# Optimization experiments

Hardware: AMD Instinct MI355X
Metric: run time of the kernel (lower is better)

Reference implementation:

```python
import jax, jax.numpy as jnp
import numpy as np

# Static config mirroring init_kwargs
B, N = 1, 5
DS = 4                      # downsample
IMG_H, IMG_W = 256 // DS, 704 // DS          # 64, 176
D0, DSTEP, ND = 1.0, 0.5, 88                 # depth grid [1, 45, 0.5]
X, Y, Z = 200, 200, 16                       # occ grid dims from x/y/z bounds
NUM_CLASS = 10
IGNORE = 9
XYZ_MIN = np.array([-100.0, -100.0, -3.0], np.float32)   # bounds in cell units
XYZ_MAX = np.array([100.0, 100.0, 13.0], np.float32)
OCC_RATIO = 2.5             # 1 / grid_size (0.4)


def _frustum():
    # matches torch.meshgrid(w, h, d, indexing='xy') -> shape (IMG_H, IMG_W, ND)
    h = jnp.arange(IMG_H, dtype=jnp.float32) + 0.5
    w = jnp.arange(IMG_W, dtype=jnp.float32) + 0.5
    d = D0 + DSTEP * jnp.arange(ND, dtype=jnp.float32)
    Hm, Wm, Dm = jnp.meshgrid(w, h, d, indexing='xy')
    return jnp.stack([Hm, Wm, Dm], axis=-1).reshape(-1, 3)  # (P, 3): x_pix, y_pix, depth


def _forward(cam2ego_rot, cam2ego_trans, cam2img, post_rots, post_trans, sem_OCC_map):
    coords = _frustum()                       # (P, 3)
    P = coords.shape[0]
    pix = jnp.concatenate([coords[:, :2], jnp.ones((P, 1), jnp.float32)], axis=1).T  # (3, P)
    ds = jnp.array([DS, DS, 1.0], jnp.float32).reshape(3, 1)
    # frustum -> camera pixel plane (undo image augmentation)
    cam_pts = pix[None, None] * ds - post_trans[..., None]                # (B,N,3,P)
    cam_pts = jnp.einsum('bnij,bnjp->bnip', jnp.linalg.inv(post_rots), cam_pts)
    # lift by depth and unproject
    cam_pts = cam_pts * coords[:, 2][None, None, None, :]
    cam_pts = jnp.einsum('bnij,bnjp->bnip', jnp.linalg.inv(cam2img), cam_pts)
    # camera -> ego
    ego = jnp.einsum('bnij,bnjp->bnip', cam2ego_rot, cam_pts) + cam2ego_trans[..., None]  # (B,N,3,P)

    ego_occ = ego * OCC_RATIO                 # ego coords in occ-cell units
    xyz_min = jnp.asarray(XYZ_MIN).reshape(1, 1, 3, 1)
    xyz_max = jnp.asarray(XYZ_MAX).reshape(1, 1, 3, 1)
    norm = (ego_occ - xyz_min) / (xyz_max - xyz_min) * 2.0 - 1.0
    occ_mask = jnp.all((norm >= -1.0) & (norm <= 1.0), axis=2)            # (B,N,P)

    grid = ego_occ - xyz_min                  # index-space coords (B,N,3,P)
    # semantic volume: softmax then argmax over class dim
    sem_idx = jnp.argmax(jax.nn.softmax(sem_OCC_map, axis=-1), axis=-1).astype(jnp.int32)  # (B,X,Y,Z)
    ix = jnp.clip(jnp.floor(grid[:, :, 0]).astype(jnp.int32), 0, X - 1)
    iy = jnp.clip(jnp.floor(grid[:, :, 1]).astype(jnp.int32), 0, Y - 1)
    iz = jnp.clip(jnp.floor(grid[:, :, 2]).astype(jnp.int32), 0, Z - 1)
    lin = (ix * Y + iy) * Z + iz                                           # (B,N,P)
    gathered = jnp.take_along_axis(sem_idx.reshape(B, -1), lin.reshape(B, -1), axis=1)
    gathered = gathered.reshape(B, N, P)
    render = jnp.where(occ_mask, gathered, IGNORE).reshape(B, N, IMG_H, IMG_W, ND)

    # first non-ignore value along depth
    first_idx = jnp.argmax((render != IGNORE).astype(jnp.int32), axis=-1)  # (B,N,H,W)
    sem_view = jnp.take_along_axis(render, first_idx[..., None], axis=-1)[..., 0]
    depth_map = D0 + DSTEP * first_idx.astype(jnp.float32)
    return sem_view, depth_map


def setup_inputs() -> dict:
    rng = np.random.default_rng(0)
    # camera looks along ego +x: rotation mapping cam z->ego x, cam x->-ego y, cam y->-ego z
    R0 = np.array([[0., 0., 1.], [-1., 0., 0.], [0., -1., 0.]], np.float32)
    cam2ego_rot = np.broadcast_to(R0, (B, N, 3, 3)).copy()
    cam2ego_rot += 0.01 * rng.standard_normal((B, N, 3, 3)).astype(np.float32)
    cam2ego_trans = (0.5 * rng.standard_normal((B, N, 3))).astype(np.float32)
    K = np.zeros((B, N, 3, 3), np.float32)
    K[..., 0, 0] = 700.0; K[..., 1, 1] = 700.0
    K[..., 0, 2] = 352.0; K[..., 1, 2] = 128.0; K[..., 2, 2] = 1.0
    post_rots = np.broadcast_to(np.eye(3, dtype=np.float32), (B, N, 3, 3)).copy()
    post_rots += 0.01 * rng.standard_normal((B, N, 3, 3)).astype(np.float32)
    post_trans = (0.1 * rng.standard_normal((B, N, 3))).astype(np.float32)
    bda = np.broadcast_to(np.eye(3, dtype=np.float32), (B, 3, 3)).copy()
    sem_OCC_map = rng.standard_normal((B, X, Y, Z, NUM_CLASS)).astype(np.float32)
    sem_view_map = rng.integers(0, NUM_CLASS, size=(B, N, IMG_H, IMG_W)).astype(np.int32)
    occ_score = rng.standard_normal((B, X, Y, Z)).astype(np.float32)
    d = dict(cam2ego_rot=cam2ego_rot, cam2ego_trans=cam2ego_trans, cam2img=K,
             post_rots=post_rots, post_trans=post_trans, bda=bda,
             sem_OCC_map=sem_OCC_map, sem_view_map=sem_view_map, occ_score=occ_score)
    return {k: jnp.asarray(v) for k, v in d.items()}


def reference(cam2ego_rot, cam2ego_trans, cam2img, post_rots, post_trans, bda,
              sem_OCC_map, sem_view_map, occ_score):
    return _forward(cam2ego_rot, cam2ego_trans, cam2img, post_rots, post_trans, sem_OCC_map)
```

## Files before the change

### kernel.cpp

```cpp
#include <hip/hip_runtime.h>


#define IMG_H 64
#define IMG_W 176
#define NCAM  5
#define NDEPTH 88
#define XDIM 200
#define YDIM 200
#define ZDIM 16
#define NCLS 10
#define IGN  9
#define PPC  (IMG_H * IMG_W)
#define SENT 0x7FFFFFFF
#define LANES 4

__device__ __forceinline__ float dot3(const float r[3], float v0, float v1, float v2) {
    return __fadd_rn(__fadd_rn(__fmul_rn(r[0], v0), __fmul_rn(r[1], v1)),
                     __fmul_rn(r[2], v2));
}

__device__ void inv3x3_gesv(const float* __restrict__ m, float out[3][3]) {
    float a[3][3];
    #pragma unroll
    for (int r = 0; r < 3; ++r)
        #pragma unroll
        for (int c = 0; c < 3; ++c)
            a[r][c] = m[r * 3 + c];

    int piv0, piv1;
    {
        int p = 0; float mx = fabsf(a[0][0]);
        if (fabsf(a[1][0]) > mx) { mx = fabsf(a[1][0]); p = 1; }
        if (fabsf(a[2][0]) > mx) { p = 2; }
        piv0 = p;
        if (p != 0) {
            #pragma unroll
            for (int c = 0; c < 3; ++c) { float t = a[0][c]; a[0][c] = a[p][c]; a[p][c] = t; }
        }
        float r0 = __fdiv_rn(1.0f, a[0][0]);
        a[1][0] = __fmul_rn(a[1][0], r0);
        a[2][0] = __fmul_rn(a[2][0], r0);
        #pragma unroll
        for (int j = 1; j < 3; ++j) {
            float t = -a[0][j];
            a[1][j] = __fadd_rn(a[1][j], __fmul_rn(a[1][0], t));
            a[2][j] = __fadd_rn(a[2][j], __fmul_rn(a[2][0], t));
        }
    }
    {
        int p = 1; float mx = fabsf(a[1][1]);
        if (fabsf(a[2][1]) > mx) { p = 2; }
        piv1 = p;
        if (p != 1) {
            #pragma unroll
            for (int c = 0; c < 3; ++c) { float t = a[1][c]; a[1][c] = a[2][c]; a[2][c] = t; }
        }
        float r1 = __fdiv_rn(1.0f, a[1][1]);
        a[2][1] = __fmul_rn(a[2][1], r1);
        a[2][2] = __fadd_rn(a[2][2], __fmul_rn(a[2][1], -a[1][2]));
    }

    float iu0 = __fdiv_rn(1.0f, a[0][0]);
    float iu1 = __fdiv_rn(1.0f, a[1][1]);
    float iu2 = __fdiv_rn(1.0f, a[2][2]);

    #pragma unroll
    for (int k = 0; k < 3; ++k) {
        float b[3] = {0.0f, 0.0f, 0.0f};
        b[k] = 1.0f;
        { float t = b[0]; b[0] = b[piv0]; b[piv0] = t; }
        { float t = b[1]; b[1] = b[piv1]; b[piv1] = t; }
        b[1] = __fsub_rn(b[1], __fmul_rn(b[0], a[1][0]));
        b[2] = __fsub_rn(b[2], __fmul_rn(b[0], a[2][0]));
        b[2] = __fsub_rn(b[2], __fmul_rn(b[1], a[2][1]));
        b[2] = __fmul_rn(b[2], iu2);
        b[1] = __fsub_rn(b[1], __fmul_rn(b[2], a[1][2]));
        b[0] = __fsub_rn(b[0], __fmul_rn(b[2], a[0][2]));
        b[1] = __fmul_rn(b[1], iu1);
        b[0] = __fsub_rn(b[0], __fmul_rn(b[1], a[0][1]));
        b[0] = __fmul_rn(b[0], iu0);
        out[0][k] = b[0];
        out[1][k] = b[1];
        out[2][k] = b[2];
    }
}

__global__ __launch_bounds__(256)
void raycast_kernel(const float* __restrict__ c2e_rot,
                    const float* __restrict__ c2e_trans,
                    const float* __restrict__ cam2img,
                    const float* __restrict__ post_rots,
                    const float* __restrict__ post_trans,
                    const float* __restrict__ sem_map,
                    float* __restrict__ out) {
    int tid = blockIdx.x * 256 + threadIdx.x;
    int g = tid >> 2;
    int l = tid & (LANES - 1);
    int n   = g / PPC;
    int rem = g - n * PPC;
    int h   = rem / IMG_W;
    int w   = rem - h * IMG_W;

    float iPR[3][3], iK[3][3], R[3][3];
    inv3x3_gesv(post_rots + n * 9, iPR);
    inv3x3_gesv(cam2img  + n * 9, iK);
    #pragma unroll
    for (int i = 0; i < 3; ++i)
        #pragma unroll
        for (int j = 0; j < 3; ++j)
            R[i][j] = c2e_rot[n * 9 + i * 3 + j];
    float tx  = c2e_trans[n * 3 + 0], ty  = c2e_trans[n * 3 + 1], tz  = c2e_trans[n * 3 + 2];
    float tp0 = post_trans[n * 3 + 0], tp1 = post_trans[n * 3 + 1], tp2 = post_trans[n * 3 + 2];

    float x = (float)w + 0.5f;
    float y = (float)h + 0.5f;
    float v0 = __fsub_rn(__fmul_rn(4.0f, x), tp0);
    float v1 = __fsub_rn(__fmul_rn(4.0f, y), tp1);
    float v2 = __fsub_rn(1.0f, tp2);
    float a0 = dot3(iPR[0], v0, v1, v2);
    float a1 = dot3(iPR[1], v0, v1, v2);
    float a2 = dot3(iPR[2], v0, v1, v2);

    int  code = SENT;
    bool seen = false;

    #pragma unroll 1
    for (int j = 0; j < NDEPTH / LANES; ++j) {
        int k = j * LANES + l;
        float d  = __fadd_rn(1.0f, __fmul_rn(0.5f, (float)k));
        float b0 = __fmul_rn(a0, d);
        float b1 = __fmul_rn(a1, d);
        float b2 = __fmul_rn(a2, d);
        float c0 = dot3(iK[0], b0, b1, b2);
        float c1 = dot3(iK[1], b0, b1, b2);
        float c2 = dot3(iK[2], b0, b1, b2);
        float e0 = __fadd_rn(dot3(R[0], c0, c1, c2), tx);
        float e1 = __fadd_rn(dot3(R[1], c0, c1, c2), ty);
        float e2 = __fadd_rn(dot3(R[2], c0, c1, c2), tz);
        float g0 = __fsub_rn(__fmul_rn(e0, 2.5f), -100.0f);
        float g1 = __fsub_rn(__fmul_rn(e1, 2.5f), -100.0f);
        float g2 = __fsub_rn(__fmul_rn(e2, 2.5f), -3.0f);
        float n0 = __fsub_rn(__fmul_rn(__fdiv_rn(g0, 200.0f), 2.0f), 1.0f);
        float n1 = __fsub_rn(__fmul_rn(__fdiv_rn(g1, 200.0f), 2.0f), 1.0f);
        float n2 = __fsub_rn(__fmul_rn(__fdiv_rn(g2, 16.0f),  2.0f), 1.0f);
        bool inb = (n0 >= -1.0f) && (n0 <= 1.0f) &&
                   (n1 >= -1.0f) && (n1 <= 1.0f) &&
                   (n2 >= -1.0f) && (n2 <= 1.0f);
        int my = SENT;
        if (inb) {
            int ix = min(max((int)floorf(g0), 0), XDIM - 1);
            int iy = min(max((int)floorf(g1), 0), YDIM - 1);
            int iz = min(max((int)floorf(g2), 0), ZDIM - 1);
            const float2* p2 = (const float2*)(sem_map + (size_t)((ix * YDIM + iy) * ZDIM + iz) * NCLS);
            float pv[NCLS];
            #pragma unroll
            for (int q = 0; q < 5; ++q) {
                float2 f = p2[q];
                pv[2 * q]     = f.x;
                pv[2 * q + 1] = f.y;
            }
            float best = pv[0];
            int   bi   = 0;
            #pragma unroll
            for (int c = 1; c < NCLS; ++c) {
                if (pv[c] > best) { best = pv[c]; bi = c; }
            }
            if (bi != IGN) my = (k << 8) | bi;
        }
        int ginb = inb ? 1 : 0;
        ginb |= __shfl_xor(ginb, 1, LANES);
        ginb |= __shfl_xor(ginb, 2, LANES);
        my = min(my, __shfl_xor(my, 1, LANES));
        my = min(my, __shfl_xor(my, 2, LANES));
        if (my != SENT) { code = my; break; }
        if (ginb) seen = true;
        else if (seen) break;
    }

    if (l == 0) {
        int oi = (n * IMG_H + h) * IMG_W + w;
        if (code != SENT) {
            int k = code >> 8;
            out[oi] = (float)(code & 255);
            out[NCAM * PPC + oi] = __fadd_rn(1.0f, __fmul_rn(0.5f, (float)k));
        } else {
            out[oi] = (float)IGN;
            out[NCAM * PPC + oi] = 1.0f;
        }
    }
}

extern "C" void kernel_launch(void* const* d_in, const int* in_sizes, int n_in,
                              void* d_out, int out_size, void* d_ws, size_t ws_size,
                              hipStream_t stream) {
    const float* c2e_rot    = (const float*)d_in[0];
    const float* c2e_trans  = (const float*)d_in[1];
    const float* cam2img    = (const float*)d_in[2];
    const float* post_rots  = (const float*)d_in[3];
    const float* post_trans = (const float*)d_in[4];
    const float* sem_map    = (const float*)d_in[6];
    float* out = (float*)d_out;

    const int total_threads = NCAM * PPC * LANES;
    raycast_kernel<<<total_threads / 256, 256, 0, stream>>>(
        c2e_rot, c2e_trans, cam2img, post_rots, post_trans, sem_map, out);
}
```

Measured before the change: 13.65 us.

## Widen depth lanes to eight per pixel and share matrix inverses per block

Each pixel's depth search is now split across 8 lanes instead of 4, which shortens the serial per-thread depth loop and adds a third shuffle stage to the lane reductions. Per-camera matrix inversions and parameter loads now run once per block on a few threads and are shared through LDS behind a barrier, instead of every thread repeating them. This removes redundant inversion arithmetic. It doubles the thread count and makes lanes do more speculative gathers past the first hit, and the barrier serialises the inversion before any thread can start. The code relies on each block of 32 pixels falling inside one camera, which holds because PPC is a multiple of 32.

```diff
diff --git a/kernel.cpp b/kernel.cpp
--- a/kernel.cpp
+++ b/kernel.cpp
@@ -12,14 +12,15 @@
 #define IGN  9
 #define PPC  (IMG_H * IMG_W)
 #define SENT 0x7FFFFFFF
-#define LANES 4
+#define LANES 8
+#define PIX_PER_BLK (256 / LANES)
 
 __device__ __forceinline__ float dot3(const float r[3], float v0, float v1, float v2) {
     return __fadd_rn(__fadd_rn(__fmul_rn(r[0], v0), __fmul_rn(r[1], v1)),
                      __fmul_rn(r[2], v2));
 }
 
-__device__ void inv3x3_gesv(const float* __restrict__ m, float out[3][3]) {
+__device__ void inv3x3_gesv(const float* __restrict__ m, float* __restrict__ out9) {
     float a[3][3];
     #pragma unroll
     for (int r = 0; r < 3; ++r)
@@ -79,9 +80,9 @@
         b[1] = __fmul_rn(b[1], iu1);
         b[0] = __fsub_rn(b[0], __fmul_rn(b[1], a[0][1]));
         b[0] = __fmul_rn(b[0], iu0);
-        out[0][k] = b[0];
-        out[1][k] = b[1];
-        out[2][k] = b[2];
+        out9[0 * 3 + k] = b[0];
+        out9[1 * 3 + k] = b[1];
+        out9[2 * 3 + k] = b[2];
     }
 }
 
@@ -93,24 +94,36 @@
                     const float* __restrict__ post_trans,
                     const float* __restrict__ sem_map,
                     float* __restrict__ out) {
+    const int n = (int)((blockIdx.x * PIX_PER_BLK) / PPC);
+
+    __shared__ float s_iPR[9], s_iK[9], s_R[9], s_t[6];
+
+    int lt = threadIdx.x;
+    if (lt == 0) inv3x3_gesv(post_rots + n * 9, s_iPR);
+    else if (lt == 1) inv3x3_gesv(cam2img + n * 9, s_iK);
+    else if (lt >= 2 && lt < 11) s_R[lt - 2] = c2e_rot[n * 9 + (lt - 2)];
+    else if (lt >= 11 && lt < 14) s_t[lt - 11] = c2e_trans[n * 3 + (lt - 11)];
+    else if (lt >= 14 && lt < 17) s_t[3 + lt - 14] = post_trans[n * 3 + (lt - 14)];
+    __syncthreads();
+
+    float iPR[3][3], iK[3][3], R[3][3];
+    #pragma unroll
+    for (int i = 0; i < 3; ++i)
+        #pragma unroll
+        for (int j = 0; j < 3; ++j) {
+            iPR[i][j] = s_iPR[i * 3 + j];
+            iK[i][j]  = s_iK[i * 3 + j];
+            R[i][j]   = s_R[i * 3 + j];
+        }
+    float tx  = s_t[0], ty  = s_t[1], tz  = s_t[2];
+    float tp0 = s_t[3], tp1 = s_t[4], tp2 = s_t[5];
+
     int tid = blockIdx.x * 256 + threadIdx.x;
-    int g = tid >> 2;
+    int g = tid / LANES;
     int l = tid & (LANES - 1);
-    int n   = g / PPC;
     int rem = g - n * PPC;
     int h   = rem / IMG_W;
     int w   = rem - h * IMG_W;
-
-    float iPR[3][3], iK[3][3], R[3][3];
-    inv3x3_gesv(post_rots + n * 9, iPR);
-    inv3x3_gesv(cam2img  + n * 9, iK);
-    #pragma unroll
-    for (int i = 0; i < 3; ++i)
-        #pragma unroll
-        for (int j = 0; j < 3; ++j)
-            R[i][j] = c2e_rot[n * 9 + i * 3 + j];
-    float tx  = c2e_trans[n * 3 + 0], ty  = c2e_trans[n * 3 + 1], tz  = c2e_trans[n * 3 + 2];
-    float tp0 = post_trans[n * 3 + 0], tp1 = post_trans[n * 3 + 1], tp2 = post_trans[n * 3 + 2];
 
     float x = (float)w + 0.5f;
     float y = (float)h + 0.5f;
@@ -170,8 +183,10 @@
         int ginb = inb ? 1 : 0;
         ginb |= __shfl_xor(ginb, 1, LANES);
         ginb |= __shfl_xor(ginb, 2, LANES);
+        ginb |= __shfl_xor(ginb, 4, LANES);
         my = min(my, __shfl_xor(my, 1, LANES));
         my = min(my, __shfl_xor(my, 2, LANES));
+        my = min(my, __shfl_xor(my, 4, LANES));
         if (my != SENT) { code = my; break; }
         if (ginb) seen = true;
         else if (seen) break;
```

Result: faster. 11.57 us (-15.3%).
